# Optimization experiments

Hardware: AMD Instinct MI355X
Metric: run time of the kernel (lower is better)

## Reference

```python
import jax, jax.numpy as jnp
import numpy as np

NFRAME = 256
NHOP = 128
BANDS = [0, 4, 8, 12, 16, 20, 24, 28, 32, 40, 44, 48, 52, 56, 64, 72, 80, 88, 96, 104, 112, 128]
NBANDS = 22


def _constants():
    F_bins = NFRAME // 2 + 1
    # sqrt-hann (periodic) analysis window
    n = np.arange(NFRAME)
    win = np.sqrt(0.5 * (1.0 - np.cos(2.0 * np.pi * n / NFRAME))).astype(np.float32)
    # triangular band filterbank matrix [NBANDS, F_bins]
    W = np.zeros((NBANDS, F_bins), np.float32)
    s, e = BANDS[0], BANDS[1]
    W[0, s:e] = 2.0 * (1.0 - np.arange(0, 1, 1.0 / (e - s)))
    s, e = BANDS[-2], BANDS[-1]
    W[-1, s:e] = 2.0 * np.arange(0, 1, 1.0 / (e - s))
    for i, (m, s, e) in enumerate(zip(BANDS[1:-1], BANDS[:-2], BANDS[2:])):
        W[i + 1, s:m] = np.arange(0, 1, 1.0 / (m - s))
        W[i + 1, m:e] = 1.0 - np.arange(0, 1, 1.0 / (e - m))
    # DCT-II matrix [NBANDS, NBANDS]
    nn = np.arange(NBANDS)
    kk = nn[:, None]
    dct = np.cos(np.pi / NBANDS * (nn + 0.5) * kk)
    dct[0] *= 1.0 / np.sqrt(2.0)
    dct *= np.sqrt(2.0 / NBANDS)
    return win, W, dct.astype(np.float32)


def setup_inputs() -> dict:
    key = jax.random.key(0)
    x = jax.random.normal(key, (32, 960000), dtype=jnp.float32)
    return {"x": x}


def reference(x):
    win, W, dct = _constants()
    B, L = x.shape
    chunks = x.reshape(B, L // NHOP, NHOP)
    frames = jnp.concatenate([chunks[:, :-1], chunks[:, 1:]], axis=-1)  # B,T,NFRAME
    frames = frames * jnp.asarray(win)
    spec = jnp.fft.rfft(frames, axis=-1)                # B,T,F complex
    pw = spec.real ** 2 + spec.imag ** 2                # |X|^2 = xk.pow(2).sum(1)
    bands_pow = jnp.einsum('btf,kf->btk', pw, jnp.asarray(W))  # fused filterbank
    feat = jnp.log10(bands_pow) @ jnp.asarray(dct).T    # B,T,22
    return feat
```

## Files before the change

kernel.cpp:

```cpp
#include <hip/hip_runtime.h>

#define NB 22
#define NFR_B 7499
#define BATCH 32
#define ROWLEN 960000
#define NFTOT (BATCH * NFR_B)

typedef float f2 __attribute__((ext_vector_type(2)));

__constant__ int c_bands[NB] = {0,4,8,12,16,20,24,28,32,40,44,48,52,56,64,72,80,88,96,104,112,128};

#define XDPP(x, CTRL) __int_as_float(__builtin_amdgcn_update_dpp(0, __float_as_int(x), CTRL, 0xF, 0xF, true))
#define XSWZ(x, PATT) __int_as_float(__builtin_amdgcn_ds_swizzle(__float_as_int(x), PATT))
#define E0S(x) XDPP(x, 0xB1)
#define E1S(x) XDPP(x, 0x4E)
#define E2S(x) XSWZ(x, 0x101F)
#define E3S(x) XDPP(x, 0x128)
#define BC32(x, B) XSWZ(x, ((B) << 5))

__device__ __forceinline__ float bperm(int addr4, float v) {
    return __int_as_float(__builtin_amdgcn_ds_bpermute(addr4, __float_as_int(v)));
}
struct fpair { float A, B; };
__device__ __forceinline__ fpair bh16(float v) {
    const unsigned u = __float_as_uint(v);
    const auto p = __builtin_amdgcn_permlane16_swap(u, u, false, false);
    fpair r; r.A = __uint_as_float(p[0]); r.B = __uint_as_float(p[1]); return r;
}
__device__ __forceinline__ fpair bh32(float v) {
    const unsigned u = __float_as_uint(v);
    const auto p = __builtin_amdgcn_permlane32_swap(u, u, false, false);
    fpair r; r.A = __uint_as_float(p[0]); r.B = __uint_as_float(p[1]); return r;
}
__device__ __forceinline__ f2 mk2(float v) { f2 r; r.x = v; r.y = v; return r; }
__device__ __forceinline__ f2 ex0v(f2 v) { f2 r; r.x = E0S(v.x); r.y = E0S(v.y); return r; }
__device__ __forceinline__ f2 ex1v(f2 v) { f2 r; r.x = E1S(v.x); r.y = E1S(v.y); return r; }
__device__ __forceinline__ f2 ex2v(f2 v) { f2 r; r.x = E2S(v.x); r.y = E2S(v.y); return r; }
__device__ __forceinline__ f2 ex3v(f2 v) { f2 r; r.x = E3S(v.x); r.y = E3S(v.y); return r; }
__device__ __forceinline__ f2 bpermv(int addr4, f2 v) {
    f2 r; r.x = bperm(addr4, v.x); r.y = bperm(addr4, v.y); return r;
}

#define PSTAGE(S, EXF)                                                    \
  { const f2 exr_a = EXF(ar2), exi_a = EXF(ai2);                          \
    const f2 exr_b = EXF(br2), exi_b = EXF(bi2);                          \
    const f2 w1r = mk2(W1r[S]), w1i = mk2(W1i[S]);                        \
    const f2 w2r = mk2(W2r[S]), w2i = mk2(W2i[S]);                        \
    const f2 nar = w1r*ar2 - w1i*ai2 + w2r*exr_a - w2i*exi_a;             \
    const f2 nai = w1r*ai2 + w1i*ar2 + w2r*exi_a + w2i*exr_a;             \
    const f2 nbr = w1r*br2 - w1i*bi2 + w2r*exr_b - w2i*exi_b;             \
    const f2 nbi = w1r*bi2 + w1i*br2 + w2r*exi_b + w2i*exr_b;             \
    ar2 = nar; ai2 = nai; br2 = nbr; bi2 = nbi; }

#define BHSTAGE(BH, WSR, WSI)                                             \
  { const fpair arx = BH(ar2.x), ary = BH(ar2.y);                         \
    const fpair aix = BH(ai2.x), aiy = BH(ai2.y);                         \
    const fpair brx = BH(br2.x), bry = BH(br2.y);                         \
    const fpair bix = BH(bi2.x), biy = BH(bi2.y);                         \
    const f2 Aar = { arx.A, ary.A }, Bar = { arx.B, ary.B };              \
    const f2 Aai = { aix.A, aiy.A }, Bai = { aix.B, aiy.B };              \
    const f2 Abr = { brx.A, bry.A }, Bbr = { brx.B, bry.B };              \
    const f2 Abi = { bix.A, biy.A }, Bbi = { bix.B, biy.B };              \
    const f2 wr = mk2(WSR), wi = mk2(WSI);                                \
    ar2 = Aar + wr*Bar - wi*Bai;                                          \
    ai2 = Aai + wr*Bai + wi*Bar;                                          \
    br2 = Abr + wr*Bbr - wi*Bbi;                                          \
    bi2 = Abi + wr*Bbi + wi*Bbr; }

#define DCTPAIR(B, ACC)                                                   \
  { const float zlo = BC32(Z, B);                                         \
    const float zhi = BC32(Z, 21 - (B));                                  \
    ACC = fmaf(coef[B], fmaf(sOc, zhi, zlo), ACC); }

__global__ __launch_bounds__(256, 4)
void feat_kernel(const float* __restrict__ x, float* __restrict__ out) {
    const int lane = threadIdx.x & 63;
    const int wid  = threadIdx.x >> 6;
    const int gwave  = blockIdx.x * (blockDim.x >> 6) + wid;
    const int nwaves = gridDim.x * (blockDim.x >> 6);

    const float PI = 3.14159265358979323846f;

    const int r = (int)(__brev((unsigned)lane) >> 25);

    float winv[4];
    #pragma unroll
    for (int j = 0; j < 4; ++j) winv[j] = sinf(PI * (float)(2 * r + j) / 256.0f);

    float W1r[4], W1i[4], W2r[4], W2i[4];
    #pragma unroll
    for (int s = 1; s < 4; ++s) {
        const int m = 1 << s;
        const float ang = -PI * (float)(lane & (m - 1)) / (float)m;
        const float wr = cosf(ang), wi = sinf(ang);
        const bool up = ((lane >> s) & 1) != 0;
        W1r[s] = up ? -wr : 1.0f;
        W1i[s] = up ? -wi : 0.0f;
        W2r[s] = up ? 1.0f : wr;
        W2i[s] = up ? 0.0f : wi;
    }
    const float sgn0 = (lane & 1) ? -1.0f : 1.0f;
    const float sg4 = ((lane >> 4) & 1) ? -1.0f : 1.0f;
    const float ang4 = -PI * (float)(lane & 15) / 16.0f;
    const float ws4r = sg4 * cosf(ang4), ws4i = sg4 * sinf(ang4);
    const float sg5 = ((lane >> 5) & 1) ? -1.0f : 1.0f;
    const float ang5 = -PI * (float)(lane & 31) / 32.0f;
    const float ws5r = sg5 * cosf(ang5), ws5i = sg5 * sinf(ang5);

    const float w6r = cosf(-PI * (float)lane / 64.0f);
    const float w6i = sinf(-PI * (float)lane / 64.0f);
    const float c1 = cosf(PI * (float)lane / 128.0f);
    const float s1 = sinf(PI * (float)lane / 128.0f);

    int seg1 = 0;
    for (int j = 1; j < 14; ++j) if (lane >= c_bands[j]) seg1 = j;
    const int wd1 = c_bands[seg1 + 1] - c_bands[seg1];
    const float a1 = (float)(lane - c_bands[seg1]) / (float)wd1;
    const float m8 = (wd1 == 8) ? 1.0f : 0.0f;
    const int bin2 = lane + 64;
    int seg2 = 14;
    for (int j = 15; j < 21; ++j) if (bin2 >= c_bands[j]) seg2 = j;
    const int wd2 = c_bands[seg2 + 1] - c_bands[seg2];
    const float a2 = (float)(bin2 - c_bands[seg2]) / (float)wd2;
    const float m16 = (seg2 == 20) ? 1.0f : 0.0f;

    const int c = lane;
    int idxA = 0; bool selA1 = true;
    if (c >= 1 && c <= 21) {
        if (c - 1 <= 13) { idxA = c_bands[c - 1]; selA1 = true; }
        else             { idxA = c_bands[c - 1] - 64; selA1 = false; }
    }
    int idxD = 0; bool selD1 = true;
    if (c <= 20) {
        if (c <= 13) { idxD = c_bands[c]; selD1 = true; }
        else         { idxD = c_bands[c] - 64; selD1 = false; }
    }
    const int bpA = idxA << 2;
    const int bpD = idxD << 2;
    const int bpHerm = (((64 - lane) & 63) << 2);

    const int oc = lane & 31;
    float coef[11];
    {
        const float norm = 0.30102999566398120f * sqrtf(2.0f / (float)NB) *
                           ((oc == 0) ? 0.70710678118654752f : 1.0f);
        #pragma unroll
        for (int b = 0; b < 11; ++b)
            coef[b] = norm * cosf(PI / (float)NB * ((float)b + 0.5f) * (float)oc);
    }
    const float sOc = (oc & 1) ? -1.0f : 1.0f;
    const float accInit = (oc == 0) ? (-2.0f * 0.30102999566398120f * sqrtf(22.0f)) : 0.0f;

    auto pipeline = [&](const float4& va, const float4& vb) -> float {
        f2 ar2 = { va.x * winv[0], vb.x * winv[0] };
        f2 ai2 = { va.y * winv[1], vb.y * winv[1] };
        f2 br2 = { va.z * winv[2], vb.z * winv[2] };
        f2 bi2 = { va.w * winv[3], vb.w * winv[3] };

        {
            const f2 e_ar = ex0v(ar2), e_ai = ex0v(ai2);
            const f2 e_br = ex0v(br2), e_bi = ex0v(bi2);
            const f2 s2 = mk2(sgn0);
            ar2 = s2 * ar2 + e_ar;  ai2 = s2 * ai2 + e_ai;
            br2 = s2 * br2 + e_br;  bi2 = s2 * bi2 + e_bi;
        }
        PSTAGE(1, ex1v)
        PSTAGE(2, ex2v)
        PSTAGE(3, ex3v)
        BHSTAGE(bh16, ws4r, ws4i)
        BHSTAGE(bh32, ws5r, ws5i)

        {
            const f2 tr2 = mk2(w6r) * br2 - mk2(w6i) * bi2;
            const f2 ti2 = mk2(w6r) * bi2 + mk2(w6i) * br2;
            const f2 nar = ar2 + tr2, nai = ai2 + ti2;
            br2 = ar2 - tr2; bi2 = ai2 - ti2;
            ar2 = nar; ai2 = nai;
        }

        const f2 par2 = bpermv(bpHerm, ar2), pai2 = bpermv(bpHerm, ai2);
        const f2 pbr2 = bpermv(bpHerm, br2), pbi2 = bpermv(bpHerm, bi2);
        const f2 P1r = (lane == 0) ? par2 : pbr2, P1i = (lane == 0) ? pai2 : pbi2;
        const f2 P2r = (lane == 0) ? pbr2 : par2, P2i = (lane == 0) ? pbi2 : pai2;

        f2 Er = ar2 + P1r, Ei = ai2 - P1i;
        f2 Or_ = ar2 - P1r, Oi = ai2 + P1i;
        const f2 X1r = Er + mk2(c1) * Oi - mk2(s1) * Or_;
        const f2 X1i = Ei - mk2(c1) * Or_ - mk2(s1) * Oi;
        const f2 pw1 = X1r * X1r + X1i * X1i;

        Er = br2 + P2r; Ei = bi2 - P2i;
        Or_ = br2 - P2r; Oi = bi2 + P2i;
        const f2 X2r = Er - mk2(s1) * Oi - mk2(c1) * Or_;
        const f2 X2i = Ei + mk2(s1) * Or_ - mk2(c1) * Oi;
        const f2 pw2 = X2r * X2r + X2i * X2i;

        f2 S1 = pw1, T1 = mk2(a1) * pw1;
        S1 = S1 + ex0v(S1); T1 = T1 + ex0v(T1);
        S1 = S1 + ex1v(S1); T1 = T1 + ex1v(T1);
        S1 = mk2(m8) * ex2v(S1) + S1; T1 = mk2(m8) * ex2v(T1) + T1;
        const f2 D1 = S1 - T1;
        f2 S2 = pw2, T2 = mk2(a2) * pw2;
        S2 = S2 + ex0v(S2); T2 = T2 + ex0v(T2);
        S2 = S2 + ex1v(S2); T2 = T2 + ex1v(T2);
        S2 = S2 + ex2v(S2); T2 = T2 + ex2v(T2);
        S2 = mk2(m16) * ex3v(S2) + S2; T2 = mk2(m16) * ex3v(T2) + T2;
        const f2 D2 = S2 - T2;

        const f2 gA1 = bpermv(bpA, T1), gA2 = bpermv(bpA, T2);
        const f2 gD1 = bpermv(bpD, D1), gD2 = bpermv(bpD, D2);
        const f2 A_prev = selA1 ? gA1 : gA2;
        const f2 D_cur  = selD1 ? gD1 : gD2;
        f2 band = A_prev + D_cur;
        if (c == 0)  band = D_cur + D_cur;
        if (c == 21) band = A_prev + A_prev;

        f2 l2;
        l2.x = __log2f(band.x);
        l2.y = __log2f(band.y);

        const fpair zsw = bh32(l2.y);
        const float Z = (lane < 32) ? l2.x : zsw.A;

        float acc0 = accInit, acc1 = 0.0f;
        DCTPAIR(0, acc0)  DCTPAIR(1, acc1)
        DCTPAIR(2, acc0)  DCTPAIR(3, acc1)
        DCTPAIR(4, acc0)  DCTPAIR(5, acc1)
        DCTPAIR(6, acc0)  DCTPAIR(7, acc1)
        DCTPAIR(8, acc0)  DCTPAIR(9, acc1)
        DCTPAIR(10, acc0)
        return acc0 + acc1;
    };

    const int chunk = (((NFTOT + nwaves - 1) / nwaves) + 3) & ~3;
    int f0 = gwave * chunk;
    if (f0 >= NFTOT) return;
    int f1 = f0 + chunk; if (f1 > NFTOT) f1 = NFTOT;
    const int f0u = __builtin_amdgcn_readfirstlane(f0);
    const int f1u = __builtin_amdgcn_readfirstlane(f1);

    int bb = f0u / NFR_B;
    int t0 = f0u - bb * NFR_B;
    const float* p0 = x + (size_t)bb * ROWLEN + (size_t)t0 * 128;
    int t1 = t0 + 1; const float* p1 = p0 + 128; if (t1 == NFR_B) { t1 = 0; p1 += 128; }
    int t2 = t1 + 1; const float* p2 = p1 + 128; if (t2 == NFR_B) { t2 = 0; p2 += 128; }
    int t3 = t2 + 1; const float* p3 = p2 + 128; if (t3 == NFR_B) { t3 = 0; p3 += 128; }

    float* ob = out + (size_t)f0u * NB + ((lane < 32) ? oc : (NB + oc));

    float4 v0 = *(const float4*)(p0 + 2 * r);
    float4 v1 = *(const float4*)(p1 + 2 * r);
    float4 v2 = *(const float4*)(p2 + 2 * r);
    float4 v3 = *(const float4*)(p3 + 2 * r);

    for (int f = f0u; f < f1u; f += 4) {
        int nt0 = t3 + 1; const float* np0 = p3 + 128; if (nt0 == NFR_B) { nt0 = 0; np0 += 128; }
        int nt1 = nt0 + 1; const float* np1 = np0 + 128; if (nt1 == NFR_B) { nt1 = 0; np1 += 128; }
        int nt2 = nt1 + 1; const float* np2 = np1 + 128; if (nt2 == NFR_B) { nt2 = 0; np2 += 128; }
        int nt3 = nt2 + 1; const float* np3 = np2 + 128; if (nt3 == NFR_B) { nt3 = 0; np3 += 128; }
        float4 nv0 = v0, nv1 = v1, nv2 = v2, nv3 = v3;
        if (f + 4 < f1u) {
            nv0 = *(const float4*)(np0 + 2 * r);
            nv1 = *(const float4*)(np1 + 2 * r);
            nv2 = *(const float4*)(np2 + 2 * r);
            nv3 = *(const float4*)(np3 + 2 * r);
        }

        const float accP = pipeline(v0, v1);
        const float accQ = pipeline(v2, v3);

        if (oc < NB) {
            ob[0]      = accP;
            ob[2 * NB] = accQ;
        }

        v0 = nv0; v1 = nv1; v2 = nv2; v3 = nv3;
        t0 = nt0; t1 = nt1; t2 = nt2; t3 = nt3;
        p0 = np0; p1 = np1; p2 = np2; p3 = np3;
        ob += 4 * NB;
    }
}

extern "C" void kernel_launch(void* const* d_in, const int* in_sizes, int n_in,
                              void* d_out, int out_size, void* d_ws, size_t ws_size,
                              hipStream_t stream) {
    const float* x = (const float*)d_in[0];
    float* out = (float*)d_out;
    feat_kernel<<<1536, 256, 0, stream>>>(x, out);
}
```

Measured before the change: 89.21 us.

## Process four frames per pipeline pass and rework DCT gather with bpermute

Widens the per-wave FFT pipeline from two frames per vector to four, so a single cross-lane FFT/filterbank pass handles all four loaded frames and the two pipeline calls become one. The DCT stage now uses a mirrored-pair pre-combination followed by per-lane ds_bpermute gathers with sign-folded coefficients, replacing the uniform swizzle broadcasts. Launch bounds are loosened to 3 blocks per SIMD and the grid is shrunk to 1024 blocks. The aim is more instruction-level parallelism per cross-lane op, at the cost of higher register pressure and lower occupancy, and the bpermute gathers go through LDS hardware.

```diff
diff --git a/kernel.cpp b/kernel.cpp
--- a/kernel.cpp
+++ b/kernel.cpp
@@ -6,7 +6,7 @@
 #define ROWLEN 960000
 #define NFTOT (BATCH * NFR_B)
 
-typedef float f2 __attribute__((ext_vector_type(2)));
+typedef float f4 __attribute__((ext_vector_type(4)));
 
 __constant__ int c_bands[NB] = {0,4,8,12,16,20,24,28,32,40,44,48,52,56,64,72,80,88,96,104,112,128};
 
@@ -16,7 +16,6 @@
 #define E1S(x) XDPP(x, 0x4E)
 #define E2S(x) XSWZ(x, 0x101F)
 #define E3S(x) XDPP(x, 0x128)
-#define BC32(x, B) XSWZ(x, ((B) << 5))
 
 __device__ __forceinline__ float bperm(int addr4, float v) {
     return __int_as_float(__builtin_amdgcn_ds_bpermute(addr4, __float_as_int(v)));
@@ -32,47 +31,46 @@
     const auto p = __builtin_amdgcn_permlane32_swap(u, u, false, false);
     fpair r; r.A = __uint_as_float(p[0]); r.B = __uint_as_float(p[1]); return r;
 }
-__device__ __forceinline__ f2 mk2(float v) { f2 r; r.x = v; r.y = v; return r; }
-__device__ __forceinline__ f2 ex0v(f2 v) { f2 r; r.x = E0S(v.x); r.y = E0S(v.y); return r; }
-__device__ __forceinline__ f2 ex1v(f2 v) { f2 r; r.x = E1S(v.x); r.y = E1S(v.y); return r; }
-__device__ __forceinline__ f2 ex2v(f2 v) { f2 r; r.x = E2S(v.x); r.y = E2S(v.y); return r; }
-__device__ __forceinline__ f2 ex3v(f2 v) { f2 r; r.x = E3S(v.x); r.y = E3S(v.y); return r; }
-__device__ __forceinline__ f2 bpermv(int addr4, f2 v) {
-    f2 r; r.x = bperm(addr4, v.x); r.y = bperm(addr4, v.y); return r;
+struct fpair4 { f4 A, B; };
+__device__ __forceinline__ fpair4 bh16v(f4 v) {
+    const fpair p0 = bh16(v.x), p1 = bh16(v.y), p2 = bh16(v.z), p3 = bh16(v.w);
+    fpair4 r; r.A = (f4){p0.A, p1.A, p2.A, p3.A}; r.B = (f4){p0.B, p1.B, p2.B, p3.B}; return r;
+}
+__device__ __forceinline__ fpair4 bh32v(f4 v) {
+    const fpair p0 = bh32(v.x), p1 = bh32(v.y), p2 = bh32(v.z), p3 = bh32(v.w);
+    fpair4 r; r.A = (f4){p0.A, p1.A, p2.A, p3.A}; r.B = (f4){p0.B, p1.B, p2.B, p3.B}; return r;
+}
+__device__ __forceinline__ f4 mk4(float v) { f4 r; r.x = v; r.y = v; r.z = v; r.w = v; return r; }
+__device__ __forceinline__ f4 ex0v(f4 v) { f4 r; r.x = E0S(v.x); r.y = E0S(v.y); r.z = E0S(v.z); r.w = E0S(v.w); return r; }
+__device__ __forceinline__ f4 ex1v(f4 v) { f4 r; r.x = E1S(v.x); r.y = E1S(v.y); r.z = E1S(v.z); r.w = E1S(v.w); return r; }
+__device__ __forceinline__ f4 ex2v(f4 v) { f4 r; r.x = E2S(v.x); r.y = E2S(v.y); r.z = E2S(v.z); r.w = E2S(v.w); return r; }
+__device__ __forceinline__ f4 ex3v(f4 v) { f4 r; r.x = E3S(v.x); r.y = E3S(v.y); r.z = E3S(v.z); r.w = E3S(v.w); return r; }
+__device__ __forceinline__ f4 bpermv(int addr4, f4 v) {
+    f4 r; r.x = bperm(addr4, v.x); r.y = bperm(addr4, v.y);
+    r.z = bperm(addr4, v.z); r.w = bperm(addr4, v.w); return r;
 }
 
 #define PSTAGE(S, EXF)                                                    \
-  { const f2 exr_a = EXF(ar2), exi_a = EXF(ai2);                          \
-    const f2 exr_b = EXF(br2), exi_b = EXF(bi2);                          \
-    const f2 w1r = mk2(W1r[S]), w1i = mk2(W1i[S]);                        \
-    const f2 w2r = mk2(W2r[S]), w2i = mk2(W2i[S]);                        \
-    const f2 nar = w1r*ar2 - w1i*ai2 + w2r*exr_a - w2i*exi_a;             \
-    const f2 nai = w1r*ai2 + w1i*ar2 + w2r*exi_a + w2i*exr_a;             \
-    const f2 nbr = w1r*br2 - w1i*bi2 + w2r*exr_b - w2i*exi_b;             \
-    const f2 nbi = w1r*bi2 + w1i*br2 + w2r*exi_b + w2i*exr_b;             \
+  { const f4 exr_a = EXF(ar2), exi_a = EXF(ai2);                          \
+    const f4 exr_b = EXF(br2), exi_b = EXF(bi2);                          \
+    const f4 w1r = mk4(W1r[S]), w1i = mk4(W1i[S]);                        \
+    const f4 w2r = mk4(W2r[S]), w2i = mk4(W2i[S]);                        \
+    const f4 nar = w1r*ar2 - w1i*ai2 + w2r*exr_a - w2i*exi_a;             \
+    const f4 nai = w1r*ai2 + w1i*ar2 + w2r*exi_a + w2i*exr_a;             \
+    const f4 nbr = w1r*br2 - w1i*bi2 + w2r*exr_b - w2i*exi_b;             \
+    const f4 nbi = w1r*bi2 + w1i*br2 + w2r*exi_b + w2i*exr_b;             \
     ar2 = nar; ai2 = nai; br2 = nbr; bi2 = nbi; }
 
-#define BHSTAGE(BH, WSR, WSI)                                             \
-  { const fpair arx = BH(ar2.x), ary = BH(ar2.y);                         \
-    const fpair aix = BH(ai2.x), aiy = BH(ai2.y);                         \
-    const fpair brx = BH(br2.x), bry = BH(br2.y);                         \
-    const fpair bix = BH(bi2.x), biy = BH(bi2.y);                         \
-    const f2 Aar = { arx.A, ary.A }, Bar = { arx.B, ary.B };              \
-    const f2 Aai = { aix.A, aiy.A }, Bai = { aix.B, aiy.B };              \
-    const f2 Abr = { brx.A, bry.A }, Bbr = { brx.B, bry.B };              \
-    const f2 Abi = { bix.A, biy.A }, Bbi = { bix.B, biy.B };              \
-    const f2 wr = mk2(WSR), wi = mk2(WSI);                                \
-    ar2 = Aar + wr*Bar - wi*Bai;                                          \
-    ai2 = Aai + wr*Bai + wi*Bar;                                          \
-    br2 = Abr + wr*Bbr - wi*Bbi;                                          \
-    bi2 = Abi + wr*Bbi + wi*Bbr; }
-
-#define DCTPAIR(B, ACC)                                                   \
-  { const float zlo = BC32(Z, B);                                         \
-    const float zhi = BC32(Z, 21 - (B));                                  \
-    ACC = fmaf(coef[B], fmaf(sOc, zhi, zlo), ACC); }
-
-__global__ __launch_bounds__(256, 4)
+#define BHSTAGE(BHV, WSR, WSI)                                            \
+  { const fpair4 par = BHV(ar2), pai = BHV(ai2);                          \
+    const fpair4 pbr = BHV(br2), pbi = BHV(bi2);                          \
+    const f4 wr = mk4(WSR), wi = mk4(WSI);                                \
+    ar2 = par.A + wr*par.B - wi*pai.B;                                    \
+    ai2 = pai.A + wr*pai.B + wi*par.B;                                    \
+    br2 = pbr.A + wr*pbr.B - wi*pbi.B;                                    \
+    bi2 = pbi.A + wr*pbi.B + wi*pbr.B; }
+
+__global__ __launch_bounds__(256, 3)
 void feat_kernel(const float* __restrict__ x, float* __restrict__ out) {
     const int lane = threadIdx.x & 63;
     const int wid  = threadIdx.x >> 6;
@@ -140,97 +138,24 @@
     const int bpHerm = (((64 - lane) & 63) << 2);
 
     const int oc = lane & 31;
-    float coef[11];
+    const int halfbase = (lane & 32) << 2;
+    float cc[11];
+    int bpB[11];
     {
         const float norm = 0.30102999566398120f * sqrtf(2.0f / (float)NB) *
                            ((oc == 0) ? 0.70710678118654752f : 1.0f);
+        const bool odd = (oc & 1) != 0;
         #pragma unroll
-        for (int b = 0; b < 11; ++b)
-            coef[b] = norm * cosf(PI / (float)NB * ((float)b + 0.5f) * (float)oc);
-    }
-    const float sOc = (oc & 1) ? -1.0f : 1.0f;
+        for (int b = 0; b < 11; ++b) {
+            const float cf = norm * cosf(PI / (float)NB * ((float)b + 0.5f) * (float)oc);
+            cc[b] = odd ? -cf : cf;
+            bpB[b] = halfbase | ((odd ? (21 - b) : b) << 2);
+        }
+    }
+    const int mir = (oc <= 21) ? (21 - oc) : 0;
+    const int bpMir = halfbase | (mir << 2);
+    const float sgnP = (oc <= 10) ? 1.0f : -1.0f;
     const float accInit = (oc == 0) ? (-2.0f * 0.30102999566398120f * sqrtf(22.0f)) : 0.0f;
-
-    auto pipeline = [&](const float4& va, const float4& vb) -> float {
-        f2 ar2 = { va.x * winv[0], vb.x * winv[0] };
-        f2 ai2 = { va.y * winv[1], vb.y * winv[1] };
-        f2 br2 = { va.z * winv[2], vb.z * winv[2] };
-        f2 bi2 = { va.w * winv[3], vb.w * winv[3] };
-
-        {
-            const f2 e_ar = ex0v(ar2), e_ai = ex0v(ai2);
-            const f2 e_br = ex0v(br2), e_bi = ex0v(bi2);
-            const f2 s2 = mk2(sgn0);
-            ar2 = s2 * ar2 + e_ar;  ai2 = s2 * ai2 + e_ai;
-            br2 = s2 * br2 + e_br;  bi2 = s2 * bi2 + e_bi;
-        }
-        PSTAGE(1, ex1v)
-        PSTAGE(2, ex2v)
-        PSTAGE(3, ex3v)
-        BHSTAGE(bh16, ws4r, ws4i)
-        BHSTAGE(bh32, ws5r, ws5i)
-
-        {
-            const f2 tr2 = mk2(w6r) * br2 - mk2(w6i) * bi2;
-            const f2 ti2 = mk2(w6r) * bi2 + mk2(w6i) * br2;
-            const f2 nar = ar2 + tr2, nai = ai2 + ti2;
-            br2 = ar2 - tr2; bi2 = ai2 - ti2;
-            ar2 = nar; ai2 = nai;
-        }
-
-        const f2 par2 = bpermv(bpHerm, ar2), pai2 = bpermv(bpHerm, ai2);
-        const f2 pbr2 = bpermv(bpHerm, br2), pbi2 = bpermv(bpHerm, bi2);
-        const f2 P1r = (lane == 0) ? par2 : pbr2, P1i = (lane == 0) ? pai2 : pbi2;
-        const f2 P2r = (lane == 0) ? pbr2 : par2, P2i = (lane == 0) ? pbi2 : pai2;
-
-        f2 Er = ar2 + P1r, Ei = ai2 - P1i;
-        f2 Or_ = ar2 - P1r, Oi = ai2 + P1i;
-        const f2 X1r = Er + mk2(c1) * Oi - mk2(s1) * Or_;
-        const f2 X1i = Ei - mk2(c1) * Or_ - mk2(s1) * Oi;
-        const f2 pw1 = X1r * X1r + X1i * X1i;
-
-        Er = br2 + P2r; Ei = bi2 - P2i;
-        Or_ = br2 - P2r; Oi = bi2 + P2i;
-        const f2 X2r = Er - mk2(s1) * Oi - mk2(c1) * Or_;
-        const f2 X2i = Ei + mk2(s1) * Or_ - mk2(c1) * Oi;
-        const f2 pw2 = X2r * X2r + X2i * X2i;
-
-        f2 S1 = pw1, T1 = mk2(a1) * pw1;
-        S1 = S1 + ex0v(S1); T1 = T1 + ex0v(T1);
-        S1 = S1 + ex1v(S1); T1 = T1 + ex1v(T1);
-        S1 = mk2(m8) * ex2v(S1) + S1; T1 = mk2(m8) * ex2v(T1) + T1;
-        const f2 D1 = S1 - T1;
-        f2 S2 = pw2, T2 = mk2(a2) * pw2;
-        S2 = S2 + ex0v(S2); T2 = T2 + ex0v(T2);
-        S2 = S2 + ex1v(S2); T2 = T2 + ex1v(T2);
-        S2 = S2 + ex2v(S2); T2 = T2 + ex2v(T2);
-        S2 = mk2(m16) * ex3v(S2) + S2; T2 = mk2(m16) * ex3v(T2) + T2;
-        const f2 D2 = S2 - T2;
-
-        const f2 gA1 = bpermv(bpA, T1), gA2 = bpermv(bpA, T2);
-        const f2 gD1 = bpermv(bpD, D1), gD2 = bpermv(bpD, D2);
-        const f2 A_prev = selA1 ? gA1 : gA2;
-        const f2 D_cur  = selD1 ? gD1 : gD2;
-        f2 band = A_prev + D_cur;
-        if (c == 0)  band = D_cur + D_cur;
-        if (c == 21) band = A_prev + A_prev;
-
-        f2 l2;
-        l2.x = __log2f(band.x);
-        l2.y = __log2f(band.y);
-
-        const fpair zsw = bh32(l2.y);
-        const float Z = (lane < 32) ? l2.x : zsw.A;
-
-        float acc0 = accInit, acc1 = 0.0f;
-        DCTPAIR(0, acc0)  DCTPAIR(1, acc1)
-        DCTPAIR(2, acc0)  DCTPAIR(3, acc1)
-        DCTPAIR(4, acc0)  DCTPAIR(5, acc1)
-        DCTPAIR(6, acc0)  DCTPAIR(7, acc1)
-        DCTPAIR(8, acc0)  DCTPAIR(9, acc1)
-        DCTPAIR(10, acc0)
-        return acc0 + acc1;
-    };
 
     const int chunk = (((NFTOT + nwaves - 1) / nwaves) + 3) & ~3;
     int f0 = gwave * chunk;
@@ -266,12 +191,101 @@
             nv3 = *(const float4*)(np3 + 2 * r);
         }
 
-        const float accP = pipeline(v0, v1);
-        const float accQ = pipeline(v2, v3);
-
-        if (oc < NB) {
-            ob[0]      = accP;
-            ob[2 * NB] = accQ;
+        f4 ar2 = { v0.x * winv[0], v1.x * winv[0], v2.x * winv[0], v3.x * winv[0] };
+        f4 ai2 = { v0.y * winv[1], v1.y * winv[1], v2.y * winv[1], v3.y * winv[1] };
+        f4 br2 = { v0.z * winv[2], v1.z * winv[2], v2.z * winv[2], v3.z * winv[2] };
+        f4 bi2 = { v0.w * winv[3], v1.w * winv[3], v2.w * winv[3], v3.w * winv[3] };
+
+        {
+            const f4 e_ar = ex0v(ar2), e_ai = ex0v(ai2);
+            const f4 e_br = ex0v(br2), e_bi = ex0v(bi2);
+            const f4 s2 = mk4(sgn0);
+            ar2 = s2 * ar2 + e_ar;  ai2 = s2 * ai2 + e_ai;
+            br2 = s2 * br2 + e_br;  bi2 = s2 * bi2 + e_bi;
+        }
+        PSTAGE(1, ex1v)
+        PSTAGE(2, ex2v)
+        PSTAGE(3, ex3v)
+        BHSTAGE(bh16v, ws4r, ws4i)
+        BHSTAGE(bh32v, ws5r, ws5i)
+
+        {
+            const f4 tr2 = mk4(w6r) * br2 - mk4(w6i) * bi2;
+            const f4 ti2 = mk4(w6r) * bi2 + mk4(w6i) * br2;
+            const f4 nar = ar2 + tr2, nai = ai2 + ti2;
+            br2 = ar2 - tr2; bi2 = ai2 - ti2;
+            ar2 = nar; ai2 = nai;
+        }
+
+        const f4 par2 = bpermv(bpHerm, ar2), pai2 = bpermv(bpHerm, ai2);
+        const f4 pbr2 = bpermv(bpHerm, br2), pbi2 = bpermv(bpHerm, bi2);
+        const f4 P1r = (lane == 0) ? par2 : pbr2, P1i = (lane == 0) ? pai2 : pbi2;
+        const f4 P2r = (lane == 0) ? pbr2 : par2, P2i = (lane == 0) ? pbi2 : pai2;
+
+        f4 Er = ar2 + P1r, Ei = ai2 - P1i;
+        f4 Or_ = ar2 - P1r, Oi = ai2 + P1i;
+        const f4 X1r = Er + mk4(c1) * Oi - mk4(s1) * Or_;
+        const f4 X1i = Ei - mk4(c1) * Or_ - mk4(s1) * Oi;
+        const f4 pw1 = X1r * X1r + X1i * X1i;
+
+        Er = br2 + P2r; Ei = bi2 - P2i;
+        Or_ = br2 - P2r; Oi = bi2 + P2i;
+        const f4 X2r = Er - mk4(s1) * Oi - mk4(c1) * Or_;
+        const f4 X2i = Ei + mk4(s1) * Or_ - mk4(c1) * Oi;
+        const f4 pw2 = X2r * X2r + X2i * X2i;
+
+        f4 S1 = pw1, T1 = mk4(a1) * pw1;
+        S1 = S1 + ex0v(S1); T1 = T1 + ex0v(T1);
+        S1 = S1 + ex1v(S1); T1 = T1 + ex1v(T1);
+        S1 = mk4(m8) * ex2v(S1) + S1; T1 = mk4(m8) * ex2v(T1) + T1;
+        const f4 D1 = S1 - T1;
+        f4 S2 = pw2, T2 = mk4(a2) * pw2;
+        S2 = S2 + ex0v(S2); T2 = T2 + ex0v(T2);
+        S2 = S2 + ex1v(S2); T2 = T2 + ex1v(T2);
+        S2 = S2 + ex2v(S2); T2 = T2 + ex2v(T2);
+        S2 = mk4(m16) * ex3v(S2) + S2; T2 = mk4(m16) * ex3v(T2) + T2;
+        const f4 D2 = S2 - T2;
+
+        const f4 gA1 = bpermv(bpA, T1), gA2 = bpermv(bpA, T2);
+        const f4 gD1 = bpermv(bpD, D1), gD2 = bpermv(bpD, D2);
+        const f4 A_prev = selA1 ? gA1 : gA2;
+        const f4 D_cur  = selD1 ? gD1 : gD2;
+        f4 band = A_prev + D_cur;
+        if (c == 0)  band = D_cur + D_cur;
+        if (c == 21) band = A_prev + A_prev;
+
+        f4 l2;
+        l2.x = __log2f(band.x);
+        l2.y = __log2f(band.y);
+        l2.z = __log2f(band.z);
+        l2.w = __log2f(band.w);
+
+        {
+            const fpair zswA = bh32(l2.y);
+            const float ZA = (lane < 32) ? l2.x : zswA.A;
+            const fpair zswB = bh32(l2.w);
+            const float ZB = (lane < 32) ? l2.z : zswB.A;
+
+            const float zmA = bperm(bpMir, ZA);
+            const float VA = fmaf(sgnP, zmA, ZA);
+            const float zmB = bperm(bpMir, ZB);
+            const float VB = fmaf(sgnP, zmB, ZB);
+
+            float accA0 = accInit, accA1 = 0.0f;
+            float accB0 = accInit, accB1 = 0.0f;
+            #pragma unroll
+            for (int b = 0; b < 11; b += 2) {
+                accA0 = fmaf(cc[b], bperm(bpB[b], VA), accA0);
+                accB0 = fmaf(cc[b], bperm(bpB[b], VB), accB0);
+                if (b + 1 < 11) {
+                    accA1 = fmaf(cc[b + 1], bperm(bpB[b + 1], VA), accA1);
+                    accB1 = fmaf(cc[b + 1], bperm(bpB[b + 1], VB), accB1);
+                }
+            }
+            if (oc < NB) {
+                ob[0]      = accA0 + accA1;
+                ob[2 * NB] = accB0 + accB1;
+            }
         }
 
         v0 = nv0; v1 = nv1; v2 = nv2; v3 = nv3;
@@ -286,5 +300,5 @@
                               hipStream_t stream) {
     const float* x = (const float*)d_in[0];
     float* out = (float*)d_out;
-    feat_kernel<<<1536, 256, 0, stream>>>(x, out);
-}
+    feat_kernel<<<1024, 256, 0, stream>>>(x, out);
+}
```

New measurement: 116.9 us. 1.31x slower.
